# Kernel optimization log

Hardware: AMD Instinct MI355X
Metric: run time of the kernel (lower is better)

## Reference

```python
import jax, jax.numpy as jnp
import numpy as np

BATCH = 2048
OUT_DIM = 50257                      # output_dim = input feature dim
LEVELS = 2
LEVEL_SIZE = int(np.ceil(OUT_DIM ** (1.0 / LEVELS)))  # 225


def setup_inputs() -> dict:
    key = jax.random.key(0)
    k_x, k_w0, k_w1 = jax.random.split(key, 3)
    # glorot-ish scale for weights so softmax logits are well behaved
    w_scale = (2.0 / (OUT_DIM + LEVEL_SIZE)) ** 0.5
    return {
        "x": jax.random.normal(k_x, (BATCH, OUT_DIM), dtype=jnp.float32),
        "W0": jax.random.normal(k_w0, (OUT_DIM, LEVEL_SIZE), dtype=jnp.float32) * w_scale,
        "W1": jax.random.normal(k_w1, (OUT_DIM, LEVEL_SIZE), dtype=jnp.float32) * w_scale,
        "b0": jnp.zeros((LEVEL_SIZE,), dtype=jnp.float32),
        "b1": jnp.zeros((LEVEL_SIZE,), dtype=jnp.float32),
    }


def reference(x, W0, W1, b0, b1):
    # per-level softmax heads: [B, L]
    h0 = jax.nn.softmax(x @ W0 + b0, axis=-1)
    h1 = jax.nn.softmax(x @ W1 + b1, axis=-1)
    # outer product per sample, flattened: [B, L*L] (replaces nested theano.scan)
    path = (h0[:, :, None] * h1[:, None, :]).reshape(x.shape[0], -1)
    # truncate to output_dim, as in original output[:, :self.output_dim]
    return path[:, :OUT_DIM]
```

## Files before the change

### kernel.cpp

```cpp
#include <hip/hip_runtime.h>
#include <stdint.h>
#include <math.h>


#define BATCH   2048
#define KDIM    50257
#define LSZ     225
#define HOFF    240
#define NPAD    480
#define BK      32
#define BM      128
#define NT      1571
#define TILE_B  30720
#define A_BYTES 16384
#define BUF_B   47104
#define LDS_TOT 94208
#define WSCALE  1024.0f

typedef __attribute__((ext_vector_type(8))) _Float16 f16x8;
typedef __attribute__((ext_vector_type(4))) float    f32x4;

__device__ __forceinline__ unsigned short f2h(float f) {
  return __builtin_bit_cast(unsigned short, (_Float16)f);
}
__device__ __forceinline__ int swzr(int r) { return ((r >> 1) & 3) << 4; }

__global__ __launch_bounds__(512) void hs_prep(const float* __restrict__ W0,
                                               const float* __restrict__ W1,
                                               unsigned char* __restrict__ wt) {
  const int kt = blockIdx.x;
  const int k0 = kt * BK;
  unsigned char* tb = wt + (size_t)kt * TILE_B;
  for (int idx = threadIdx.x; idx < NPAD * 8; idx += 512) {
    const int n = idx >> 3, c4 = idx & 7;
    const float* src = nullptr;
    if (n < HOFF) { if (n < LSZ) src = W0 + n; }
    else          { if (n - HOFF < LSZ) src = W1 + (n - HOFF); }
    unsigned short he[4];
#pragma unroll
    for (int e = 0; e < 4; ++e) {
      const int k = k0 + c4 * 4 + e;
      float v = (src != nullptr && k < KDIM) ? src[(size_t)k * LSZ] * WSCALE : 0.0f;
      he[e] = f2h(v);
    }
    const int jp = (c4 * 8) ^ swzr(n);
    *(ushort4*)(tb + n * 64 + jp) = make_ushort4(he[0], he[1], he[2], he[3]);
  }
}

__global__ __launch_bounds__(768, 3) void hs_gemm(
    const float* __restrict__ x, const unsigned char* __restrict__ wt,
    float* __restrict__ partials, int ksplit, int tpc) {
  extern __shared__ __align__(16) unsigned char smem[];
  const int bid   = blockIdx.x;
  const int chunk = bid % ksplit;
  const int mtile = bid / ksplit;
  const int t0 = chunk * tpc;
  int t1 = t0 + tpc; if (t1 > NT) t1 = NT;
  const int m0 = mtile * BM;
  const int tid = threadIdx.x;
  const int lane = tid & 63, wid = tid >> 6;
  const int wm = wid & 3, wn = wid >> 2;
  const int jl  = (lane >> 4) * 16;
  const int l15 = lane & 15;

  const int arow = tid >> 2, c8 = tid & 3;
  const bool astg = (tid < 512);
  const float* xr = x + (size_t)(m0 + arow) * KDIM + c8 * 8;
  const int aoff = arow * 64 + ((c8 * 16) ^ swzr(arow));

  f32x4 acc[2][10];
#pragma unroll
  for (int mf = 0; mf < 2; ++mf)
#pragma unroll
    for (int nf = 0; nf < 10; ++nf)
      acc[mf][nf] = f32x4{0.f, 0.f, 0.f, 0.f};

  auto stageB = [&](int kt, int buf) {
    const unsigned char* src = wt + (size_t)kt * TILE_B + lane * 16;
    unsigned char* dstb = smem + buf * BUF_B;
#pragma unroll
    for (int c = 0; c < 3; ++c) {
      const int cc = wid + c * 12;
      if (cc < 30) {
        __builtin_amdgcn_global_load_lds(
            (const __attribute__((address_space(1))) unsigned int*)(src + cc * 1024),
            (__attribute__((address_space(3))) unsigned int*)(dstb + cc * 1024),
            16, 0, 0);
      }
    }
  };

  auto loadA = [&](int kt, f32x4& v0, f32x4& v1) {
    if (!astg) return;
    const int kb = kt * BK + c8 * 8;
    const float* p = xr + (size_t)kt * BK;
    if (kb + 8 <= KDIM) {
      __builtin_memcpy(&v0, p, 16);
      __builtin_memcpy(&v1, p + 4, 16);
    } else {
#pragma unroll
      for (int e = 0; e < 4; ++e) {
        v0[e] = (kb + e < KDIM)     ? p[e]     : 0.f;
        v1[e] = (kb + 4 + e < KDIM) ? p[4 + e] : 0.f;
      }
    }
  };

  auto writeA = [&](int buf, const f32x4& v0, const f32x4& v1) {
    if (!astg) return;
    unsigned char* ab = smem + buf * BUF_B + TILE_B;
    unsigned short he[8], le[8];
#pragma unroll
    for (int e = 0; e < 4; ++e) {
      const _Float16 h = (_Float16)v0[e];
      he[e] = __builtin_bit_cast(unsigned short, h);
      le[e] = f2h(v0[e] - (float)h);
      const _Float16 g = (_Float16)v1[e];
      he[4 + e] = __builtin_bit_cast(unsigned short, g);
      le[4 + e] = f2h(v1[e] - (float)g);
    }
    *(ushort4*)(ab + aoff)            = make_ushort4(he[0], he[1], he[2], he[3]);
    *(ushort4*)(ab + aoff + 8)        = make_ushort4(he[4], he[5], he[6], he[7]);
    *(ushort4*)(ab + 8192 + aoff)     = make_ushort4(le[0], le[1], le[2], le[3]);
    *(ushort4*)(ab + 8192 + aoff + 8) = make_ushort4(le[4], le[5], le[6], le[7]);
  };

  auto compute = [&](int buf) {
    const unsigned char* bb = smem + buf * BUF_B;
    const unsigned char* ab = bb + TILE_B;
    f16x8 ah[2], al[2];
#pragma unroll
    for (int mf = 0; mf < 2; ++mf) {
      const int m = wm * 32 + mf * 16 + l15;
      const int off = m * 64 + (jl ^ swzr(m));
      ah[mf] = *(const f16x8*)(ab + off);
      al[mf] = *(const f16x8*)(ab + 8192 + off);
    }
#pragma unroll
    for (int nf = 0; nf < 10; ++nf) {
      const int n = wn * 160 + nf * 16 + l15;
      const int off = n * 64 + (jl ^ swzr(n));
      const f16x8 bw = *(const f16x8*)(bb + off);
#pragma unroll
      for (int mf = 0; mf < 2; ++mf) {
        acc[mf][nf] = __builtin_amdgcn_mfma_f32_16x16x32_f16(ah[mf], bw, acc[mf][nf], 0, 0, 0);
        acc[mf][nf] = __builtin_amdgcn_mfma_f32_16x16x32_f16(al[mf], bw, acc[mf][nf], 0, 0, 0);
      }
    }
  };

  if (t0 < t1) {
    f32x4 v0, v1;
    stageB(t0, 0);
    loadA(t0, v0, v1);
    writeA(0, v0, v1);
    __syncthreads();
    int buf = 0;
    for (int t = t0; t < t1; ++t) {
      const bool more = (t + 1 < t1);
      if (more) {
        stageB(t + 1, buf ^ 1);
        loadA(t + 1, v0, v1);
      }
      compute(buf);
      if (more) writeA(buf ^ 1, v0, v1);
      __syncthreads();
      buf ^= 1;
    }
  }

  float* pout = partials + ((size_t)chunk * BATCH + m0) * NPAD;
#pragma unroll
  for (int mf = 0; mf < 2; ++mf)
#pragma unroll
    for (int nf = 0; nf < 10; ++nf)
#pragma unroll
      for (int r = 0; r < 4; ++r) {
        const int row = wm * 32 + mf * 16 + (lane >> 4) * 4 + r;
        const int col = wn * 160 + nf * 16 + l15;
        pout[(size_t)row * NPAD + col] = acc[mf][nf][r];
      }
}

__global__ __launch_bounds__(512) void hs_finish(
    const float* __restrict__ partials, const float* __restrict__ b0,
    const float* __restrict__ b1, float* __restrict__ out, int ksplit) {
  const int b = blockIdx.x;
  __shared__ float lg[NPAD];
  __shared__ float red[4];
  const int tid = threadIdx.x;
  if (tid < NPAD) {
    float v = 0.f;
    for (int c = 0; c < ksplit; ++c)
      v += partials[((size_t)c * BATCH + b) * NPAD + tid];
    v *= (1.0f / WSCALE);
    if (tid < LSZ) v += b0[tid];
    else if (tid >= HOFF && tid < HOFF + LSZ) v += b1[tid - HOFF];
    lg[tid] = v;
  }
  __syncthreads();
  const int wid = tid >> 6, lane = tid & 63;
  if (wid < 2) {
    const int base = wid * HOFF;
    float m = -1e30f;
    for (int i = lane; i < LSZ; i += 64) m = fmaxf(m, lg[base + i]);
#pragma unroll
    for (int s = 32; s; s >>= 1) m = fmaxf(m, __shfl_xor(m, s));
    float sum = 0.f;
    for (int i = lane; i < LSZ; i += 64) sum += __expf(lg[base + i] - m);
#pragma unroll
    for (int s = 32; s; s >>= 1) sum += __shfl_xor(sum, s);
    if (lane == 0) { red[wid * 2] = m; red[wid * 2 + 1] = 1.0f / sum; }
  }
  __syncthreads();
  if (tid < NPAD) {
    const int h = (tid >= HOFF) ? 1 : 0;
    const int off = tid - (h ? HOFF : 0);
    float hv = 0.f;
    if (off < LSZ) hv = __expf(lg[tid] - red[2 * h]) * red[2 * h + 1];
    lg[tid] = hv;
  }
  __syncthreads();
  const size_t ob = (size_t)b * KDIM;
  for (int f = tid; f < KDIM; f += 512) {
    const int i = f / LSZ;
    const int j = f - i * LSZ;
    out[ob + f] = lg[i] * lg[HOFF + j];
  }
}

extern "C" void kernel_launch(void* const* d_in, const int* in_sizes, int n_in,
                              void* d_out, int out_size, void* d_ws, size_t ws_size,
                              hipStream_t stream) {
  (void)in_sizes; (void)n_in; (void)out_size;
  const float* x  = (const float*)d_in[0];
  const float* W0 = (const float*)d_in[1];
  const float* W1 = (const float*)d_in[2];
  const float* b0 = (const float*)d_in[3];
  const float* b1 = (const float*)d_in[4];
  float* out = (float*)d_out;
  unsigned char* ws = (unsigned char*)d_ws;

  const size_t WT_BYTES  = (size_t)NT * TILE_B;
  const size_t PER_CHUNK = (size_t)BATCH * NPAD * sizeof(float);
  int ksplit = 16;
  if (ws_size > WT_BYTES) {
    const int kmax = (int)((ws_size - WT_BYTES) / PER_CHUNK);
    if (ksplit > kmax) ksplit = kmax;
  } else {
    ksplit = 1;
  }
  if (ksplit < 1) ksplit = 1;
  float* partials = (float*)(ws + WT_BYTES);
  const int tpc = (NT + ksplit - 1) / ksplit;

  hs_prep<<<dim3(NT), dim3(512), 0, stream>>>(W0, W1, ws);
  hipFuncSetAttribute((const void*)hs_gemm,
                      hipFuncAttributeMaxDynamicSharedMemorySize, LDS_TOT);
  hs_gemm<<<dim3(16 * ksplit), dim3(768), LDS_TOT, stream>>>(x, ws, partials, ksplit, tpc);
  hs_finish<<<dim3(BATCH), dim3(512), 0, stream>>>(partials, b0, b1, out, ksplit);
}
```

Baseline: 346.3 us.

## Drop fp16 hi/lo split of x, retile warps, vectorize output stores

```diff
diff --git a/kernel.cpp b/kernel.cpp
--- a/kernel.cpp
+++ b/kernel.cpp
@@ -12,9 +12,9 @@
 #define BM      128
 #define NT      1571
 #define TILE_B  30720
-#define A_BYTES 16384
-#define BUF_B   47104
-#define LDS_TOT 94208
+#define A_BYTES 8192
+#define BUF_B   38912
+#define LDS_TOT 77824
 #define WSCALE  1024.0f
 
 typedef __attribute__((ext_vector_type(8))) _Float16 f16x8;
@@ -60,7 +60,7 @@
   const int m0 = mtile * BM;
   const int tid = threadIdx.x;
   const int lane = tid & 63, wid = tid >> 6;
-  const int wm = wid & 3, wn = wid >> 2;
+  const int wm = wid & 1, wn = wid >> 1;
   const int jl  = (lane >> 4) * 16;
   const int l15 = lane & 15;
 
@@ -69,11 +69,11 @@
   const float* xr = x + (size_t)(m0 + arow) * KDIM + c8 * 8;
   const int aoff = arow * 64 + ((c8 * 16) ^ swzr(arow));
 
-  f32x4 acc[2][10];
-#pragma unroll
-  for (int mf = 0; mf < 2; ++mf)
-#pragma unroll
-    for (int nf = 0; nf < 10; ++nf)
+  f32x4 acc[4][5];
+#pragma unroll
+  for (int mf = 0; mf < 4; ++mf)
+#pragma unroll
+    for (int nf = 0; nf < 5; ++nf)
       acc[mf][nf] = f32x4{0.f, 0.f, 0.f, 0.f};
 
   auto stageB = [&](int kt, int buf) {
@@ -110,43 +110,34 @@
   auto writeA = [&](int buf, const f32x4& v0, const f32x4& v1) {
     if (!astg) return;
     unsigned char* ab = smem + buf * BUF_B + TILE_B;
-    unsigned short he[8], le[8];
+    unsigned short he[8];
 #pragma unroll
     for (int e = 0; e < 4; ++e) {
-      const _Float16 h = (_Float16)v0[e];
-      he[e] = __builtin_bit_cast(unsigned short, h);
-      le[e] = f2h(v0[e] - (float)h);
-      const _Float16 g = (_Float16)v1[e];
-      he[4 + e] = __builtin_bit_cast(unsigned short, g);
-      le[4 + e] = f2h(v1[e] - (float)g);
-    }
-    *(ushort4*)(ab + aoff)            = make_ushort4(he[0], he[1], he[2], he[3]);
-    *(ushort4*)(ab + aoff + 8)        = make_ushort4(he[4], he[5], he[6], he[7]);
-    *(ushort4*)(ab + 8192 + aoff)     = make_ushort4(le[0], le[1], le[2], le[3]);
-    *(ushort4*)(ab + 8192 + aoff + 8) = make_ushort4(le[4], le[5], le[6], le[7]);
+      he[e]     = f2h(v0[e]);
+      he[4 + e] = f2h(v1[e]);
+    }
+    *(ushort4*)(ab + aoff)     = make_ushort4(he[0], he[1], he[2], he[3]);
+    *(ushort4*)(ab + aoff + 8) = make_ushort4(he[4], he[5], he[6], he[7]);
   };
 
   auto compute = [&](int buf) {
     const unsigned char* bb = smem + buf * BUF_B;
     const unsigned char* ab = bb + TILE_B;
-    f16x8 ah[2], al[2];
-#pragma unroll
-    for (int mf = 0; mf < 2; ++mf) {
-      const int m = wm * 32 + mf * 16 + l15;
+    f16x8 ah[4];
+#pragma unroll
+    for (int mf = 0; mf < 4; ++mf) {
+      const int m = wm * 64 + mf * 16 + l15;
       const int off = m * 64 + (jl ^ swzr(m));
       ah[mf] = *(const f16x8*)(ab + off);
-      al[mf] = *(const f16x8*)(ab + 8192 + off);
-    }
-#pragma unroll
-    for (int nf = 0; nf < 10; ++nf) {
-      const int n = wn * 160 + nf * 16 + l15;
+    }
+#pragma unroll
+    for (int nf = 0; nf < 5; ++nf) {
+      const int n = wn * 80 + nf * 16 + l15;
       const int off = n * 64 + (jl ^ swzr(n));
       const f16x8 bw = *(const f16x8*)(bb + off);
 #pragma unroll
-      for (int mf = 0; mf < 2; ++mf) {
+      for (int mf = 0; mf < 4; ++mf)
         acc[mf][nf] = __builtin_amdgcn_mfma_f32_16x16x32_f16(ah[mf], bw, acc[mf][nf], 0, 0, 0);
-        acc[mf][nf] = __builtin_amdgcn_mfma_f32_16x16x32_f16(al[mf], bw, acc[mf][nf], 0, 0, 0);
-      }
     }
   };
 
@@ -172,13 +163,13 @@
 
   float* pout = partials + ((size_t)chunk * BATCH + m0) * NPAD;
 #pragma unroll
-  for (int mf = 0; mf < 2; ++mf)
-#pragma unroll
-    for (int nf = 0; nf < 10; ++nf)
+  for (int mf = 0; mf < 4; ++mf)
+#pragma unroll
+    for (int nf = 0; nf < 5; ++nf)
 #pragma unroll
       for (int r = 0; r < 4; ++r) {
-        const int row = wm * 32 + mf * 16 + (lane >> 4) * 4 + r;
-        const int col = wn * 160 + nf * 16 + l15;
+        const int row = wm * 64 + mf * 16 + (lane >> 4) * 4 + r;
+        const int col = wn * 80 + nf * 16 + l15;
         pout[(size_t)row * NPAD + col] = acc[mf][nf][r];
       }
 }
@@ -223,7 +214,23 @@
   }
   __syncthreads();
   const size_t ob = (size_t)b * KDIM;
-  for (int f = tid; f < KDIM; f += 512) {
+  const int h4 = (4 - (b & 3)) & 3;
+  if (tid < h4) out[ob + tid] = lg[0] * lg[HOFF + tid];
+  const int nbody = (KDIM - h4) >> 2;
+  for (int q = tid; q < nbody; q += 512) {
+    const int f = h4 + q * 4;
+    int i = f / LSZ;
+    int j = f - i * LSZ;
+    float4 v;
+    v.x = lg[i] * lg[HOFF + j]; if (++j == LSZ) { j = 0; ++i; }
+    v.y = lg[i] * lg[HOFF + j]; if (++j == LSZ) { j = 0; ++i; }
+    v.z = lg[i] * lg[HOFF + j]; if (++j == LSZ) { j = 0; ++i; }
+    v.w = lg[i] * lg[HOFF + j];
+    *(float4*)(out + ob + f) = v;
+  }
+  const int be = h4 + nbody * 4;
+  if (tid < KDIM - be) {
+    const int f = be + tid;
     const int i = f / LSZ;
     const int j = f - i * LSZ;
     out[ob + f] = lg[i] * lg[HOFF + j];
```

Result: slower. 381.2 us (+10.1%).
